# Kernel optimization log

Measured on AMD Instinct MI355X. Metric: run time of the kernel, lower is better.

The kernel has to match this reference:

```python
import jax, jax.numpy as jnp
import numpy as np


def _ln(x, g, b, eps=1e-5):
    m = jnp.mean(x, axis=-1, keepdims=True)
    v = jnp.mean(jnp.square(x - m), axis=-1, keepdims=True)
    return (x - m) * jax.lax.rsqrt(v + eps) * g + b


def setup_inputs() -> dict:
    N, F, H = 1024, 256, 64
    key = jax.random.key(0)
    ks = jax.random.split(key, 24)
    r = lambda k, s, sc=0.05: jax.random.normal(k, s, jnp.float32) * sc
    return {
        "features": jax.random.normal(ks[0], (N, F), jnp.float32),
        "ip_w1": r(ks[1], (F, H)), "ip_b1": r(ks[2], (H,)),
        "ip_ln_g": jnp.ones((H,), jnp.float32), "ip_ln_b": jnp.zeros((H,), jnp.float32),
        "ip_w2": r(ks[3], (H, H)), "ip_b2": r(ks[4], (H,)),
        "attn_in_w": r(ks[5], (H, 3 * H)), "attn_in_b": r(ks[6], (3 * H,)),
        "attn_out_w": r(ks[7], (H, H)), "attn_out_b": r(ks[8], (H,)),
        "attn_ln_g": jnp.ones((H,), jnp.float32), "attn_ln_b": jnp.zeros((H,), jnp.float32),
        "pg_w1": r(ks[9], (4 * H, H)), "pg_b1": r(ks[10], (H,)),
        "pg_w2": r(ks[11], (H, 1)), "pg_b2": r(ks[12], (1,)),
        "pv_w1": r(ks[13], (4 * H, H)), "pv_b1": r(ks[14], (H,)),
        "pv_w2": r(ks[15], (H, H)), "pv_b2": r(ks[16], (H,)),
        "ctx_ln_g": jnp.ones((H,), jnp.float32), "ctx_ln_b": jnp.zeros((H,), jnp.float32),
        "sh_w1": r(ks[17], (2 * H, H)), "sh_b1": r(ks[18], (H,)),
        "sh_w2": r(ks[19], (H, 1)), "sh_b2": r(ks[20], (1,)),
    }


def reference(features, ip_w1, ip_b1, ip_ln_g, ip_ln_b, ip_w2, ip_b2,
              attn_in_w, attn_in_b, attn_out_w, attn_out_b, attn_ln_g, attn_ln_b,
              pg_w1, pg_b1, pg_w2, pg_b2, pv_w1, pv_b1, pv_w2, pv_b2,
              ctx_ln_g, ctx_ln_b, sh_w1, sh_b1, sh_w2, sh_b2):
    N = features.shape[0]
    H = ip_w1.shape[1]
    NH = 4
    HD = H // NH
    # input_proj: Linear -> LayerNorm -> ReLU -> Linear -> ReLU
    h = jax.nn.relu(_ln(features @ ip_w1 + ip_b1, ip_ln_g, ip_ln_b))
    h = jax.nn.relu(h @ ip_w2 + ip_b2)
    # MultiheadAttention (batch=1, seq=N) with residual + LayerNorm
    qkv = h @ attn_in_w + attn_in_b
    q, k, v = jnp.split(qkv, 3, axis=-1)
    q = q.reshape(N, NH, HD)
    k = k.reshape(N, NH, HD)
    v = v.reshape(N, NH, HD)
    scores = jnp.einsum('ihd,jhd->hij', q, k) / np.sqrt(HD)
    attn = jax.nn.softmax(scores, axis=-1)
    o = jnp.einsum('hij,jhd->ihd', attn, v).reshape(N, H) @ attn_out_w + attn_out_b
    enc = _ln(h + o, attn_ln_g, attn_ln_b)
    # dense all-pairs gated message passing
    lhs = jnp.broadcast_to(enc[:, None, :], (N, N, H))
    rhs = jnp.broadcast_to(enc[None, :, :], (N, N, H))
    diff = lhs - rhs
    pf = jnp.concatenate([lhs, rhs, diff, jnp.abs(diff)], axis=-1)  # [N, N, 4H]
    gates = (jax.nn.relu(pf @ pg_w1 + pg_b1) @ pg_w2 + pg_b2)[..., 0]  # [N, N]
    gates = jnp.where(jnp.eye(N, dtype=bool), jnp.float32(-1e9), gates)
    w = jax.nn.softmax(gates, axis=1)
    vals = jax.nn.relu(pf @ pv_w1 + pv_b1) @ pv_w2 + pv_b2  # [N, N, H]
    pair_context = jnp.einsum('ij,ijh->ih', w, vals)
    enc2 = _ln(enc + pair_context, ctx_ln_g, ctx_ln_b)
    # score head with mean graph context
    g = jnp.broadcast_to(jnp.mean(enc2, axis=0, keepdims=True), (N, H))
    cat = jnp.concatenate([enc2, g], axis=-1)
    return (jax.nn.relu(cat @ sh_w1 + sh_b1) @ sh_w2 + sh_b2)[..., 0]  # [N]
```

## Files before the change

kernel.cpp:

```cpp
#include <hip/hip_runtime.h>
#include <hip/hip_bf16.h>
#include <hip/hip_fp16.h>
#include <math.h>

#define N 1024
#define F 256
#define H 64

typedef __attribute__((ext_vector_type(8))) _Float16 f16x8;
typedef __attribute__((ext_vector_type(4))) unsigned int u32x4;
typedef __attribute__((ext_vector_type(4))) float f32x4;

__device__ __forceinline__ float wave_reduce_sum(float v) {
#pragma unroll
  for (int off = 32; off; off >>= 1) v += __shfl_xor(v, off, 64);
  return v;
}

__device__ __forceinline__ unsigned int hpack(float a, float b) {
  __half ha = __float2half(a), hb = __float2half(b);
  unsigned short ua = __builtin_bit_cast(unsigned short, ha);
  unsigned short ub = __builtin_bit_cast(unsigned short, hb);
  return (unsigned int)ua | ((unsigned int)ub << 16);
}

__device__ __forceinline__ unsigned int absdiff2(unsigned int a, unsigned int b) {
  __half2 ah = __builtin_bit_cast(__half2, a);
  __half2 bh = __builtin_bit_cast(__half2, b);
  __half2 d = __hsub2(ah, bh);
  return __builtin_bit_cast(unsigned int, d) & 0x7FFF7FFFu;
}

__global__ void k_input_qkv(const float* __restrict__ feat,
                            const float* __restrict__ w1, const float* __restrict__ b1,
                            const float* __restrict__ lng, const float* __restrict__ lnb,
                            const float* __restrict__ w2, const float* __restrict__ b2,
                            const float* __restrict__ aw, const float* __restrict__ abias,
                            float* __restrict__ h, float* __restrict__ Qh,
                            float* __restrict__ Kh, float* __restrict__ Vh) {
  const int row = blockIdx.x;
  const int lane = threadIdx.x;
  __shared__ float frow[F];
#pragma unroll
  for (int c = 0; c < 4; ++c) frow[c * 64 + lane] = feat[row * F + c * 64 + lane];
  __syncthreads();
  float acc = b1[lane];
#pragma unroll 8
  for (int k = 0; k < F; ++k) acc += frow[k] * w1[k * H + lane];
  float mu = wave_reduce_sum(acc) * (1.f / 64.f);
  float d = acc - mu;
  float var = wave_reduce_sum(d * d) * (1.f / 64.f);
  float y = d * rsqrtf(var + 1e-5f) * lng[lane] + lnb[lane];
  y = fmaxf(y, 0.f);
  __shared__ float yrow[H];
  yrow[lane] = y;
  __syncthreads();
  float acc2 = b2[lane];
#pragma unroll 8
  for (int k = 0; k < H; ++k) acc2 += yrow[k] * w2[k * H + lane];
  float hv = fmaxf(acc2, 0.f);
  h[row * H + lane] = hv;
  __shared__ float hrow[H];
  hrow[lane] = hv;
  __syncthreads();
  float a0 = abias[lane], a1 = abias[64 + lane], a2 = abias[128 + lane];
#pragma unroll 8
  for (int k = 0; k < H; ++k) {
    float hk = hrow[k];
    a0 += hk * aw[k * 192 + lane];
    a1 += hk * aw[k * 192 + 64 + lane];
    a2 += hk * aw[k * 192 + 128 + lane];
  }
  const int base = (lane >> 4) * (N * 16) + row * 16 + (lane & 15);
  Qh[base] = a0;
  Kh[base] = a1;
  Vh[base] = a2;
}

__global__ __launch_bounds__(256) void k_attn2(const float* __restrict__ Qh,
                                               const float* __restrict__ Kh,
                                               const float* __restrict__ Vh,
                                               float* __restrict__ o) {
  const int head = blockIdx.x >> 8;
  const int i0 = (blockIdx.x & 255) * 4;
  const int tid = threadIdx.x;
  const int q2 = tid >> 6, js = tid & 63;
  const int i = i0 + q2;

  const float* qp = Qh + head * (N * 16) + i * 16;
  const float4 q0 = *(const float4*)(qp);
  const float4 q1 = *(const float4*)(qp + 4);
  const float4 q2v = *(const float4*)(qp + 8);
  const float4 q3 = *(const float4*)(qp + 12);
  const float* kb = Kh + head * (N * 16);
  const float* vb = Vh + head * (N * 16);

  float m = -3.0e38f, s = 0.f;
  float4 c0 = {0, 0, 0, 0}, c1 = {0, 0, 0, 0}, c2 = {0, 0, 0, 0}, c3 = {0, 0, 0, 0};

  int j = js;
  const float* kp = kb + j * 16;
  const float* vp = vb + j * 16;
  float4 k0 = *(const float4*)(kp), k1 = *(const float4*)(kp + 4);
  float4 k2 = *(const float4*)(kp + 8), k3 = *(const float4*)(kp + 12);
  float4 v0 = *(const float4*)(vp), v1 = *(const float4*)(vp + 4);
  float4 v2 = *(const float4*)(vp + 8), v3 = *(const float4*)(vp + 12);

#pragma unroll 1
  for (int t = 0; t < 16; ++t) {
    const int jn = (j + 64) & (N - 1);
    const float* kpn = kb + jn * 16;
    const float* vpn = vb + jn * 16;
    float4 nk0 = *(const float4*)(kpn), nk1 = *(const float4*)(kpn + 4);
    float4 nk2 = *(const float4*)(kpn + 8), nk3 = *(const float4*)(kpn + 12);
    float4 nv0 = *(const float4*)(vpn), nv1 = *(const float4*)(vpn + 4);
    float4 nv2 = *(const float4*)(vpn + 8), nv3 = *(const float4*)(vpn + 12);

    float sc = q0.x * k0.x + q0.y * k0.y + q0.z * k0.z + q0.w * k0.w;
    sc += q1.x * k1.x + q1.y * k1.y + q1.z * k1.z + q1.w * k1.w;
    sc += q2v.x * k2.x + q2v.y * k2.y + q2v.z * k2.z + q2v.w * k2.w;
    sc += q3.x * k3.x + q3.y * k3.y + q3.z * k3.z + q3.w * k3.w;
    sc *= 0.25f;

    float mn = fmaxf(m, sc);
    float cc = __expf(m - mn);
    float p = __expf(sc - mn);
    s = s * cc + p;
    m = mn;
    c0.x = c0.x * cc + p * v0.x; c0.y = c0.y * cc + p * v0.y;
    c0.z = c0.z * cc + p * v0.z; c0.w = c0.w * cc + p * v0.w;
    c1.x = c1.x * cc + p * v1.x; c1.y = c1.y * cc + p * v1.y;
    c1.z = c1.z * cc + p * v1.z; c1.w = c1.w * cc + p * v1.w;
    c2.x = c2.x * cc + p * v2.x; c2.y = c2.y * cc + p * v2.y;
    c2.z = c2.z * cc + p * v2.z; c2.w = c2.w * cc + p * v2.w;
    c3.x = c3.x * cc + p * v3.x; c3.y = c3.y * cc + p * v3.y;
    c3.z = c3.z * cc + p * v3.z; c3.w = c3.w * cc + p * v3.w;

    k0 = nk0; k1 = nk1; k2 = nk2; k3 = nk3;
    v0 = nv0; v1 = nv1; v2 = nv2; v3 = nv3;
    j = jn;
  }

  float M = m, S = s;
#pragma unroll
  for (int off = 32; off; off >>= 1) {
    float Mo = __shfl_xor(M, off, 64);
    float So = __shfl_xor(S, off, 64);
    float Mn = fmaxf(M, Mo);
    S = S * __expf(M - Mn) + So * __expf(Mo - Mn);
    M = Mn;
  }
  const float wgt = __expf(m - M) / S;

  __shared__ float lds[4][64][17];
  float* lp = &lds[q2][js][0];
  lp[0] = c0.x * wgt;  lp[1] = c0.y * wgt;  lp[2] = c0.z * wgt;  lp[3] = c0.w * wgt;
  lp[4] = c1.x * wgt;  lp[5] = c1.y * wgt;  lp[6] = c1.z * wgt;  lp[7] = c1.w * wgt;
  lp[8] = c2.x * wgt;  lp[9] = c2.y * wgt;  lp[10] = c2.z * wgt; lp[11] = c2.w * wgt;
  lp[12] = c3.x * wgt; lp[13] = c3.y * wgt; lp[14] = c3.z * wgt; lp[15] = c3.w * wgt;
  __syncthreads();

  if (tid < 64) {
    const int q = tid >> 4, d = tid & 15;
    float sum = 0.f;
#pragma unroll
    for (int k = 0; k < 64; ++k) sum += lds[q][k][d];
    o[(i0 + q) * H + head * 16 + d] = sum;
  }
}

__global__ void k_attn_out(const float* __restrict__ o, const float* __restrict__ w,
                           const float* __restrict__ b, const float* __restrict__ h,
                           const float* __restrict__ lng, const float* __restrict__ lnb,
                           float* __restrict__ enc) {
  const int row = blockIdx.x;
  const int lane = threadIdx.x;
  __shared__ float orow[H];
  orow[lane] = o[row * H + lane];
  __syncthreads();
  float a = b[lane];
#pragma unroll 8
  for (int k = 0; k < H; ++k) a += orow[k] * w[k * H + lane];
  float x = h[row * H + lane] + a;
  float mu = wave_reduce_sum(x) * (1.f / 64.f);
  float d = x - mu;
  float var = wave_reduce_sum(d * d) * (1.f / 64.f);
  enc[row * H + lane] = d * rsqrtf(var + 1e-5f) * lng[lane] + lnb[lane];
}

__global__ __launch_bounds__(256) void k_prep(const float* __restrict__ pg1,
                                              const float* __restrict__ pv1,
                                              float* __restrict__ WgA, float* __restrict__ WgB,
                                              float* __restrict__ WvA, float* __restrict__ WvB,
                                              unsigned int* __restrict__ WF) {
  const int blk = blockIdx.x;
  if (blk < 16) {
    int idx = blk * 256 + threadIdx.x;
    float g1 = pg1[idx];
    float g2 = pg1[4096 + idx];
    float g3 = pg1[8192 + idx];
    WgA[idx] = g1 + g3;
    WgB[idx] = g2 - g3;
    float v1 = pv1[idx];
    float v2 = pv1[4096 + idx];
    float v3 = pv1[8192 + idx];
    WvA[idx] = v1 + v3;
    WvB[idx] = v2 - v3;
  } else {
    const int sub = threadIdx.x >> 6;
    const int lane = threadIdx.x & 63;
    const int b = (blk - 16) * 4 + sub;
    const float* W = (b & 8) ? pv1 : pg1;
    const int Mt = b & 3;
    const int ks = (b >> 2) & 1;
    const int l = Mt * 16 + (lane & 15);
    const int kb = 192 + ks * 32 + (lane >> 4) * 8;
    uint4 o;
    o.x = hpack(W[(kb + 0) * H + l], W[(kb + 1) * H + l]);
    o.y = hpack(W[(kb + 2) * H + l], W[(kb + 3) * H + l]);
    o.z = hpack(W[(kb + 4) * H + l], W[(kb + 5) * H + l]);
    o.w = hpack(W[(kb + 6) * H + l], W[(kb + 7) * H + l]);
    ((uint4*)WF)[b * 64 + lane] = o;
  }
}

__global__ void k_ab(const float* __restrict__ enc, const float* __restrict__ WgA,
                     const float* __restrict__ WgB, const float* __restrict__ WvA,
                     const float* __restrict__ WvB, const float* __restrict__ pg_b1,
                     const float* __restrict__ pv_b1, float* __restrict__ Ag,
                     float* __restrict__ Av, float* __restrict__ Pg,
                     float* __restrict__ Pv, unsigned int* __restrict__ encH) {
  const int row = blockIdx.x;
  const int lane = threadIdx.x;
  __shared__ float erow[H];
  erow[lane] = enc[row * H + lane];
  __syncthreads();
  if (lane < 32) encH[row * 32 + lane] = hpack(erow[2 * lane], erow[2 * lane + 1]);
  float ag = pg_b1[lane], bg = 0.f, av = pv_b1[lane], bv = 0.f;
#pragma unroll 4
  for (int k = 0; k < H; ++k) {
    float e = erow[k];
    ag += e * WgA[k * H + lane];
    bg += e * WgB[k * H + lane];
    av += e * WvA[k * H + lane];
    bv += e * WvB[k * H + lane];
  }
  Ag[row * H + lane] = ag;
  Av[row * H + lane] = av;
  int idx = (((row >> 4) * 4 + (lane >> 4)) * 4 + ((lane >> 2) & 3)) * 64 +
            (row & 15) * 4 + (lane & 3);
  Pg[idx] = bg;
  Pv[idx] = bv;
}

__global__ __launch_bounds__(128) void k_pairp(
    const unsigned int* __restrict__ encH, const float* __restrict__ Ag,
    const float* __restrict__ Av, const unsigned int* __restrict__ WF,
    const float* __restrict__ Pg, const float* __restrict__ Pv,
    const float* __restrict__ pg_w2, const float* __restrict__ pg_b2,
    float* __restrict__ Pm, float* __restrict__ Ps,
    float* __restrict__ Pctx0, float* __restrict__ Pctx1) {
  const int bid = blockIdx.x;
  const int i = bid & (N - 1);
  const int half = bid >> 10;
  const int tid = threadIdx.x;
  const int lane = tid & 63;
  const int w = tid >> 6;
  const int l15 = lane & 15, g4 = lane >> 4;
  const float LOG2E = 1.44269504088896f;

  f16x8 wg[2][4], wv[2][4];
  const uint4* WF4 = (const uint4*)WF;
#pragma unroll
  for (int ks = 0; ks < 2; ++ks)
#pragma unroll
    for (int Mt = 0; Mt < 4; ++Mt) {
      wg[ks][Mt] = __builtin_bit_cast(f16x8, WF4[(ks * 4 + Mt) * 64 + lane]);
      wv[ks][Mt] = __builtin_bit_cast(f16x8, WF4[((2 + ks) * 4 + Mt) * 64 + lane]);
    }

  const uint4* eH = (const uint4*)encH + (size_t)i * 8;
  const uint4 eiL = eH[g4];
  const uint4 eiU = eH[4 + g4];

  f32x4 agv[4], avv[4];
  float4 w2s[4];
#pragma unroll
  for (int Mt = 0; Mt < 4; ++Mt) {
    float4 t = *(const float4*)(Ag + i * H + Mt * 16 + g4 * 4);
    agv[Mt] = f32x4{t.x, t.y, t.z, t.w};
    float4 u = *(const float4*)(Av + i * H + Mt * 16 + g4 * 4);
    avv[Mt] = f32x4{u.x, u.y, u.z, u.w};
    float4 ww = *(const float4*)(pg_w2 + Mt * 16 + g4 * 4);
    w2s[Mt] = make_float4(ww.x * LOG2E, ww.y * LOG2E, ww.z * LOG2E, ww.w * LOG2E);
  }
  const float b2g = pg_b2[0] * LOG2E;

  float m = -3.0e38f, s = 0.f;
  float ctx[16];
#pragma unroll
  for (int e = 0; e < 16; ++e) ctx[e] = 0.f;

  const int jbase = half * 512 + w * 256;
  const uint4* ejp = (const uint4*)encH + (size_t)(jbase + l15) * 8;
  uint4 na = ejp[g4];
  uint4 nc = ejp[4 + g4];

#pragma unroll 1
  for (int t = 0; t < 16; ++t) {
    const int j0 = jbase + t * 16;
    const int pbase = ((j0 >> 4) * 16 + g4) * 64 + l15 * 4;
    float4 pg0 = *(const float4*)(Pg + pbase);
    float4 pg1 = *(const float4*)(Pg + pbase + 256);
    float4 pg2 = *(const float4*)(Pg + pbase + 512);
    float4 pg3 = *(const float4*)(Pg + pbase + 768);

    u32x4 t0 = {absdiff2(eiL.x, na.x), absdiff2(eiL.y, na.y),
                absdiff2(eiL.z, na.z), absdiff2(eiL.w, na.w)};
    u32x4 t1 = {absdiff2(eiU.x, nc.x), absdiff2(eiU.y, nc.y),
                absdiff2(eiU.z, nc.z), absdiff2(eiU.w, nc.w)};
    f16x8 b0 = __builtin_bit_cast(f16x8, t0);
    f16x8 b1 = __builtin_bit_cast(f16x8, t1);
    ejp += 16 * 8;
    na = ejp[g4];
    nc = ejp[4 + g4];

    f32x4 cg[4], cv[4];
#pragma unroll
    for (int Mt = 0; Mt < 4; ++Mt) {
      cg[Mt] = __builtin_amdgcn_mfma_f32_16x16x32_f16(wg[0][Mt], b0, agv[Mt], 0, 0, 0);
      cg[Mt] = __builtin_amdgcn_mfma_f32_16x16x32_f16(wg[1][Mt], b1, cg[Mt], 0, 0, 0);
      cv[Mt] = __builtin_amdgcn_mfma_f32_16x16x32_f16(wv[0][Mt], b0, avv[Mt], 0, 0, 0);
      cv[Mt] = __builtin_amdgcn_mfma_f32_16x16x32_f16(wv[1][Mt], b1, cv[Mt], 0, 0, 0);
    }

    float4 pv0 = *(const float4*)(Pv + pbase);
    float4 pv1 = *(const float4*)(Pv + pbase + 256);
    float4 pv2 = *(const float4*)(Pv + pbase + 512);
    float4 pv3 = *(const float4*)(Pv + pbase + 768);

    float ga = fmaxf(cg[0][0] + pg0.x, 0.f) * w2s[0].x;
    float gb = fmaxf(cg[0][1] + pg0.y, 0.f) * w2s[0].y;
    float gc = fmaxf(cg[0][2] + pg0.z, 0.f) * w2s[0].z;
    float gd = fmaxf(cg[0][3] + pg0.w, 0.f) * w2s[0].w;
    ga = fmaf(fmaxf(cg[1][0] + pg1.x, 0.f), w2s[1].x, ga);
    gb = fmaf(fmaxf(cg[1][1] + pg1.y, 0.f), w2s[1].y, gb);
    gc = fmaf(fmaxf(cg[1][2] + pg1.z, 0.f), w2s[1].z, gc);
    gd = fmaf(fmaxf(cg[1][3] + pg1.w, 0.f), w2s[1].w, gd);
    ga = fmaf(fmaxf(cg[2][0] + pg2.x, 0.f), w2s[2].x, ga);
    gb = fmaf(fmaxf(cg[2][1] + pg2.y, 0.f), w2s[2].y, gb);
    gc = fmaf(fmaxf(cg[2][2] + pg2.z, 0.f), w2s[2].z, gc);
    gd = fmaf(fmaxf(cg[2][3] + pg2.w, 0.f), w2s[2].w, gd);
    ga = fmaf(fmaxf(cg[3][0] + pg3.x, 0.f), w2s[3].x, ga);
    gb = fmaf(fmaxf(cg[3][1] + pg3.y, 0.f), w2s[3].y, gb);
    gc = fmaf(fmaxf(cg[3][2] + pg3.z, 0.f), w2s[3].z, gc);
    gd = fmaf(fmaxf(cg[3][3] + pg3.w, 0.f), w2s[3].w, gd);
    float gate = (ga + gb) + (gc + gd);
    gate += __shfl_xor(gate, 16, 64);
    gate += __shfl_xor(gate, 32, 64);
    gate += b2g;
    if (j0 + l15 == i) gate = -3.0e38f;

    float p;
    if (__any(gate > m + 8.f)) {
      float mn = fmaxf(m, gate);
      float c = exp2f(m - mn);
      p = exp2f(gate - mn);
      s *= c;
      m = mn;
#pragma unroll
      for (int e = 0; e < 16; ++e) ctx[e] *= c;
    } else {
      p = exp2f(gate - m);
    }
    s += p;
    ctx[0]  = fmaf(p, fmaxf(cv[0][0] + pv0.x, 0.f), ctx[0]);
    ctx[1]  = fmaf(p, fmaxf(cv[0][1] + pv0.y, 0.f), ctx[1]);
    ctx[2]  = fmaf(p, fmaxf(cv[0][2] + pv0.z, 0.f), ctx[2]);
    ctx[3]  = fmaf(p, fmaxf(cv[0][3] + pv0.w, 0.f), ctx[3]);
    ctx[4]  = fmaf(p, fmaxf(cv[1][0] + pv1.x, 0.f), ctx[4]);
    ctx[5]  = fmaf(p, fmaxf(cv[1][1] + pv1.y, 0.f), ctx[5]);
    ctx[6]  = fmaf(p, fmaxf(cv[1][2] + pv1.z, 0.f), ctx[6]);
    ctx[7]  = fmaf(p, fmaxf(cv[1][3] + pv1.w, 0.f), ctx[7]);
    ctx[8]  = fmaf(p, fmaxf(cv[2][0] + pv2.x, 0.f), ctx[8]);
    ctx[9]  = fmaf(p, fmaxf(cv[2][1] + pv2.y, 0.f), ctx[9]);
    ctx[10] = fmaf(p, fmaxf(cv[2][2] + pv2.z, 0.f), ctx[10]);
    ctx[11] = fmaf(p, fmaxf(cv[2][3] + pv2.w, 0.f), ctx[11]);
    ctx[12] = fmaf(p, fmaxf(cv[3][0] + pv3.x, 0.f), ctx[12]);
    ctx[13] = fmaf(p, fmaxf(cv[3][1] + pv3.y, 0.f), ctx[13]);
    ctx[14] = fmaf(p, fmaxf(cv[3][2] + pv3.z, 0.f), ctx[14]);
    ctx[15] = fmaf(p, fmaxf(cv[3][3] + pv3.w, 0.f), ctx[15]);
  }

#pragma unroll
  for (int off = 1; off <= 8; off <<= 1) {
    float mo = __shfl_xor(m, off, 64);
    float so = __shfl_xor(s, off, 64);
    float M2 = fmaxf(m, mo);
    float ca = exp2f(m - M2);
    float cb = exp2f(mo - M2);
    s = s * ca + so * cb;
#pragma unroll
    for (int e = 0; e < 16; ++e) {
      float co = __shfl_xor(ctx[e], off, 64);
      ctx[e] = ctx[e] * ca + co * cb;
    }
    m = M2;
  }

  __shared__ float ctxs[2][64];
  __shared__ float mss[2][2];
  if (l15 == 0) {
#pragma unroll
    for (int Mt = 0; Mt < 4; ++Mt)
#pragma unroll
      for (int r = 0; r < 4; ++r) ctxs[w][Mt * 16 + g4 * 4 + r] = ctx[Mt * 4 + r];
  }
  if (lane == 0) {
    mss[w][0] = m;
    mss[w][1] = s;
  }
  __syncthreads();

  if (w == 0) {
    float m0 = mss[0][0], s0 = mss[0][1], m1 = mss[1][0], s1 = mss[1][1];
    float M = fmaxf(m0, m1);
    float e0 = exp2f(m0 - M), e1 = exp2f(m1 - M);
    float S = s0 * e0 + s1 * e1;
    float cm = ctxs[0][lane] * e0 + ctxs[1][lane] * e1;
    float* dst = half ? Pctx1 : Pctx0;
    dst[i * H + lane] = cm;
    if (lane == 0) {
      Pm[bid] = M;
      Ps[bid] = S;
    }
  }
}

__global__ void k_pmerge(const float* __restrict__ Pm, const float* __restrict__ Ps,
                         const float* __restrict__ Pctx0, const float* __restrict__ Pctx1,
                         const float* __restrict__ enc, const float* __restrict__ pv_w2,
                         const float* __restrict__ pv_b2, const float* __restrict__ lng,
                         const float* __restrict__ lnb, float* __restrict__ enc2) {
  const int i = blockIdx.x;
  const int lane = threadIdx.x;
  float m0 = Pm[i], s0 = Ps[i], m1 = Pm[N + i], s1 = Ps[N + i];
  float c0 = Pctx0[i * H + lane];
  float c1 = Pctx1[i * H + lane];
  float M = fmaxf(m0, m1);
  float e0 = exp2f(m0 - M), e1 = exp2f(m1 - M);
  float S = s0 * e0 + s1 * e1;
  float cp = (c0 * e0 + c1 * e1) / S;
  float pc = pv_b2[lane];
#pragma unroll 8
  for (int k = 0; k < 64; ++k) pc += __shfl(cp, k, 64) * pv_w2[k * H + lane];
  float x = enc[i * H + lane] + pc;
  float mu = wave_reduce_sum(x) * (1.f / 64.f);
  float dd = x - mu;
  float var = wave_reduce_sum(dd * dd) * (1.f / 64.f);
  enc2[i * H + lane] = dd * rsqrtf(var + 1e-5f) * lng[lane] + lnb[lane];
}

__global__ __launch_bounds__(256) void k_colsum(const float* __restrict__ enc2,
                                                float* __restrict__ part) {
  const int b = blockIdx.x;
  const int lane = threadIdx.x & 63, grp = threadIdx.x >> 6;
  const float* p = enc2 + (b * 32 + grp) * H + lane;
  float s = 0.f;
#pragma unroll
  for (int r = 0; r < 8; ++r) s += p[r * 4 * H];
  __shared__ float sh[4][64];
  sh[grp][lane] = s;
  __syncthreads();
  if (grp == 0) part[b * 64 + lane] = sh[0][lane] + sh[1][lane] + sh[2][lane] + sh[3][lane];
}

__global__ void k_score(const float* __restrict__ enc2, const float* __restrict__ sh_w1,
                        const float* __restrict__ sh_b1, const float* __restrict__ sh_w2,
                        const float* __restrict__ sh_b2, const float* __restrict__ part,
                        float* __restrict__ out) {
  const int row = blockIdx.x;
  const int lane = threadIdx.x;
  __shared__ float erow[H];
  erow[lane] = enc2[row * H + lane];
  __syncthreads();
  float g = 0.f;
#pragma unroll
  for (int p = 0; p < 32; ++p) g += part[p * 64 + lane];
  g *= (1.f / N);
  float t = sh_b1[lane];
#pragma unroll 8
  for (int k = 0; k < 64; ++k) {
    t += erow[k] * sh_w1[k * H + lane];
    t += __shfl(g, k, 64) * sh_w1[(64 + k) * H + lane];
  }
  t = fmaxf(t, 0.f);
  float prt = t * sh_w2[lane];
  float sum = wave_reduce_sum(prt);
  if (lane == 0) out[row] = sum + sh_b2[0];
}

extern "C" void kernel_launch(void* const* d_in, const int* in_sizes, int n_in,
                              void* d_out, int out_size, void* d_ws, size_t ws_size,
                              hipStream_t stream) {
  const float* feat = (const float*)d_in[0];
  const float* ip_w1 = (const float*)d_in[1];
  const float* ip_b1 = (const float*)d_in[2];
  const float* ip_ln_g = (const float*)d_in[3];
  const float* ip_ln_b = (const float*)d_in[4];
  const float* ip_w2 = (const float*)d_in[5];
  const float* ip_b2 = (const float*)d_in[6];
  const float* attn_in_w = (const float*)d_in[7];
  const float* attn_in_b = (const float*)d_in[8];
  const float* attn_out_w = (const float*)d_in[9];
  const float* attn_out_b = (const float*)d_in[10];
  const float* attn_ln_g = (const float*)d_in[11];
  const float* attn_ln_b = (const float*)d_in[12];
  const float* pg_w1 = (const float*)d_in[13];
  const float* pg_b1 = (const float*)d_in[14];
  const float* pg_w2 = (const float*)d_in[15];
  const float* pg_b2 = (const float*)d_in[16];
  const float* pv_w1 = (const float*)d_in[17];
  const float* pv_b1 = (const float*)d_in[18];
  const float* pv_w2 = (const float*)d_in[19];
  const float* pv_b2 = (const float*)d_in[20];
  const float* ctx_ln_g = (const float*)d_in[21];
  const float* ctx_ln_b = (const float*)d_in[22];
  const float* sh_w1 = (const float*)d_in[23];
  const float* sh_b1 = (const float*)d_in[24];
  const float* sh_w2 = (const float*)d_in[25];
  const float* sh_b2 = (const float*)d_in[26];

  float* ws = (float*)d_ws;
  float* h = ws;
  float* Qh = ws + 65536;
  float* Kh = ws + 131072;
  float* Vh = ws + 196608;
  float* o = ws + 262144;
  float* enc = ws + 327680;
  float* enc2 = ws + 393216;
  float* Pg = ws + 65536;
  float* Pv = ws + 131072;
  float* Ag = ws + 196608;
  float* Av = ws + 262144;
  float* Pctx0 = ws;
  float* Pctx1 = enc2;
  float* WgA = ws + 458752;
  float* WgB = ws + 462848;
  float* WvA = ws + 466944;
  float* WvB = ws + 471040;
  unsigned int* WF = (unsigned int*)(ws + 475136);
  float* part = ws + 479232;
  float* Pm = ws + 481280;
  float* Ps = ws + 483328;
  unsigned int* encH = (unsigned int*)(ws + 485376);
  float* out = (float*)d_out;

  k_input_qkv<<<N, 64, 0, stream>>>(feat, ip_w1, ip_b1, ip_ln_g, ip_ln_b, ip_w2, ip_b2,
                                    attn_in_w, attn_in_b, h, Qh, Kh, Vh);
  k_attn2<<<1024, 256, 0, stream>>>(Qh, Kh, Vh, o);
  k_attn_out<<<N, 64, 0, stream>>>(o, attn_out_w, attn_out_b, h, attn_ln_g, attn_ln_b, enc);
  k_prep<<<20, 256, 0, stream>>>(pg_w1, pv_w1, WgA, WgB, WvA, WvB, WF);
  k_ab<<<N, 64, 0, stream>>>(enc, WgA, WgB, WvA, WvB, pg_b1, pv_b1, Ag, Av, Pg, Pv, encH);
  k_pairp<<<2 * N, 128, 0, stream>>>(encH, Ag, Av, WF, Pg, Pv, pg_w2, pg_b2, Pm, Ps,
                                     Pctx0, Pctx1);
  k_pmerge<<<N, 64, 0, stream>>>(Pm, Ps, Pctx0, Pctx1, enc, pv_w2, pv_b2, ctx_ln_g,
                                 ctx_ln_b, enc2);
  k_colsum<<<32, 256, 0, stream>>>(enc2, part);
  k_score<<<N, 64, 0, stream>>>(enc2, sh_w1, sh_b1, sh_w2, sh_b2, part, out);
}
```

Baseline: 107.8 us.

## Fuse small kernels, pack four rows per block, stage attention K/V in LDS

Merges the weight-prep kernel into the input/QKV kernel, attn_out into k_ab, and colsum into k_score, cutting the launch count from nine to six. The per-row kernels now run four rows per 256-thread block. The attention kernel stages K/V tiles through double-buffered shared memory instead of each thread loading its own rows from global memory. Each k_score block now recomputes the full column sum redundantly, and the workspace layout is remapped (Av and Pctx0 swap regions) to avoid overlaps.

```diff
diff --git a/kernel.cpp b/kernel.cpp
--- a/kernel.cpp
+++ b/kernel.cpp
@@ -31,42 +31,78 @@
   return __builtin_bit_cast(unsigned int, d) & 0x7FFF7FFFu;
 }
 
-__global__ void k_input_qkv(const float* __restrict__ feat,
-                            const float* __restrict__ w1, const float* __restrict__ b1,
-                            const float* __restrict__ lng, const float* __restrict__ lnb,
-                            const float* __restrict__ w2, const float* __restrict__ b2,
-                            const float* __restrict__ aw, const float* __restrict__ abias,
-                            float* __restrict__ h, float* __restrict__ Qh,
-                            float* __restrict__ Kh, float* __restrict__ Vh) {
-  const int row = blockIdx.x;
-  const int lane = threadIdx.x;
-  __shared__ float frow[F];
-#pragma unroll
-  for (int c = 0; c < 4; ++c) frow[c * 64 + lane] = feat[row * F + c * 64 + lane];
+__global__ __launch_bounds__(256) void k_input_qkv_prep(
+    const float* __restrict__ feat, const float* __restrict__ w1,
+    const float* __restrict__ b1, const float* __restrict__ lng,
+    const float* __restrict__ lnb, const float* __restrict__ w2,
+    const float* __restrict__ b2, const float* __restrict__ aw,
+    const float* __restrict__ abias, const float* __restrict__ pg1,
+    const float* __restrict__ pv1, float* __restrict__ h, float* __restrict__ Qh,
+    float* __restrict__ Kh, float* __restrict__ Vh, float* __restrict__ WgA,
+    float* __restrict__ WgB, float* __restrict__ WvA, float* __restrict__ WvB,
+    unsigned int* __restrict__ WF) {
+  if (blockIdx.x >= 256) {
+    const int pb = blockIdx.x - 256;
+    const int tid = threadIdx.x;
+#pragma unroll
+    for (int c = 0; c < 4; ++c) {
+      int idx = (pb * 4 + c) * 256 + tid;
+      float g1 = pg1[idx];
+      float g2 = pg1[4096 + idx];
+      float g3 = pg1[8192 + idx];
+      WgA[idx] = g1 + g3;
+      WgB[idx] = g2 - g3;
+      float v1 = pv1[idx];
+      float v2 = pv1[4096 + idx];
+      float v3 = pv1[8192 + idx];
+      WvA[idx] = v1 + v3;
+      WvB[idx] = v2 - v3;
+    }
+    const int sub = tid >> 6;
+    const int lane = tid & 63;
+    const int b = pb * 4 + sub;
+    const float* W = (b & 8) ? pv1 : pg1;
+    const int Mt = b & 3;
+    const int ks = (b >> 2) & 1;
+    const int l = Mt * 16 + (lane & 15);
+    const int kb = 192 + ks * 32 + (lane >> 4) * 8;
+    uint4 o;
+    o.x = hpack(W[(kb + 0) * H + l], W[(kb + 1) * H + l]);
+    o.y = hpack(W[(kb + 2) * H + l], W[(kb + 3) * H + l]);
+    o.z = hpack(W[(kb + 4) * H + l], W[(kb + 5) * H + l]);
+    o.w = hpack(W[(kb + 6) * H + l], W[(kb + 7) * H + l]);
+    ((uint4*)WF)[b * 64 + lane] = o;
+    return;
+  }
+  const int sub = threadIdx.x >> 6, lane = threadIdx.x & 63;
+  const int row = blockIdx.x * 4 + sub;
+  __shared__ float frow[4][F];
+#pragma unroll
+  for (int c = 0; c < 4; ++c) frow[sub][c * 64 + lane] = feat[row * F + c * 64 + lane];
   __syncthreads();
   float acc = b1[lane];
 #pragma unroll 8
-  for (int k = 0; k < F; ++k) acc += frow[k] * w1[k * H + lane];
+  for (int k = 0; k < F; ++k) acc += frow[sub][k] * w1[k * H + lane];
   float mu = wave_reduce_sum(acc) * (1.f / 64.f);
   float d = acc - mu;
   float var = wave_reduce_sum(d * d) * (1.f / 64.f);
   float y = d * rsqrtf(var + 1e-5f) * lng[lane] + lnb[lane];
   y = fmaxf(y, 0.f);
-  __shared__ float yrow[H];
-  yrow[lane] = y;
+  __shared__ float yrow[4][H];
+  yrow[sub][lane] = y;
   __syncthreads();
   float acc2 = b2[lane];
 #pragma unroll 8
-  for (int k = 0; k < H; ++k) acc2 += yrow[k] * w2[k * H + lane];
+  for (int k = 0; k < H; ++k) acc2 += yrow[sub][k] * w2[k * H + lane];
   float hv = fmaxf(acc2, 0.f);
   h[row * H + lane] = hv;
-  __shared__ float hrow[H];
-  hrow[lane] = hv;
+  __shared__ float hrow[4][H];
+  hrow[sub][lane] = hv;
   __syncthreads();
   float a0 = abias[lane], a1 = abias[64 + lane], a2 = abias[128 + lane];
 #pragma unroll 8
   for (int k = 0; k < H; ++k) {
-    float hk = hrow[k];
+    float hk = hrow[sub][k];
     a0 += hk * aw[k * 192 + lane];
     a1 += hk * aw[k * 192 + 64 + lane];
     a2 += hk * aw[k * 192 + 128 + lane];
@@ -95,26 +131,28 @@
   const float* kb = Kh + head * (N * 16);
   const float* vb = Vh + head * (N * 16);
 
+  __shared__ float4 kt[2][4][64];
+  __shared__ float4 vt[2][4][64];
+  const int sr = tid & 63, sg = tid >> 6;
+  kt[0][sg][sr] = *(const float4*)(kb + sr * 16 + sg * 4);
+  vt[0][sg][sr] = *(const float4*)(vb + sr * 16 + sg * 4);
+  __syncthreads();
+
   float m = -3.0e38f, s = 0.f;
   float4 c0 = {0, 0, 0, 0}, c1 = {0, 0, 0, 0}, c2 = {0, 0, 0, 0}, c3 = {0, 0, 0, 0};
 
-  int j = js;
-  const float* kp = kb + j * 16;
-  const float* vp = vb + j * 16;
-  float4 k0 = *(const float4*)(kp), k1 = *(const float4*)(kp + 4);
-  float4 k2 = *(const float4*)(kp + 8), k3 = *(const float4*)(kp + 12);
-  float4 v0 = *(const float4*)(vp), v1 = *(const float4*)(vp + 4);
-  float4 v2 = *(const float4*)(vp + 8), v3 = *(const float4*)(vp + 12);
-
 #pragma unroll 1
   for (int t = 0; t < 16; ++t) {
-    const int jn = (j + 64) & (N - 1);
-    const float* kpn = kb + jn * 16;
-    const float* vpn = vb + jn * 16;
-    float4 nk0 = *(const float4*)(kpn), nk1 = *(const float4*)(kpn + 4);
-    float4 nk2 = *(const float4*)(kpn + 8), nk3 = *(const float4*)(kpn + 12);
-    float4 nv0 = *(const float4*)(vpn), nv1 = *(const float4*)(vpn + 4);
-    float4 nv2 = *(const float4*)(vpn + 8), nv3 = *(const float4*)(vpn + 12);
+    const int cur = t & 1;
+    if (t < 15) {
+      const int jr = (t + 1) * 64 + sr;
+      kt[cur ^ 1][sg][sr] = *(const float4*)(kb + jr * 16 + sg * 4);
+      vt[cur ^ 1][sg][sr] = *(const float4*)(vb + jr * 16 + sg * 4);
+    }
+    const float4 k0 = kt[cur][0][js], k1 = kt[cur][1][js];
+    const float4 k2 = kt[cur][2][js], k3 = kt[cur][3][js];
+    const float4 v0 = vt[cur][0][js], v1 = vt[cur][1][js];
+    const float4 v2 = vt[cur][2][js], v3 = vt[cur][3][js];
 
     float sc = q0.x * k0.x + q0.y * k0.y + q0.z * k0.z + q0.w * k0.w;
     sc += q1.x * k1.x + q1.y * k1.y + q1.z * k1.z + q1.w * k1.w;
@@ -135,10 +173,7 @@
     c2.z = c2.z * cc + p * v2.z; c2.w = c2.w * cc + p * v2.w;
     c3.x = c3.x * cc + p * v3.x; c3.y = c3.y * cc + p * v3.y;
     c3.z = c3.z * cc + p * v3.z; c3.w = c3.w * cc + p * v3.w;
-
-    k0 = nk0; k1 = nk1; k2 = nk2; k3 = nk3;
-    v0 = nv0; v1 = nv1; v2 = nv2; v3 = nv3;
-    j = jn;
+    __syncthreads();
   }
 
   float M = m, S = s;
@@ -169,81 +204,41 @@
   }
 }
 
-__global__ void k_attn_out(const float* __restrict__ o, const float* __restrict__ w,
-                           const float* __restrict__ b, const float* __restrict__ h,
-                           const float* __restrict__ lng, const float* __restrict__ lnb,
-                           float* __restrict__ enc) {
-  const int row = blockIdx.x;
-  const int lane = threadIdx.x;
-  __shared__ float orow[H];
-  orow[lane] = o[row * H + lane];
+__global__ __launch_bounds__(256) void k_attn_ab(
+    const float* __restrict__ o, const float* __restrict__ w, const float* __restrict__ b,
+    const float* __restrict__ h, const float* __restrict__ lng,
+    const float* __restrict__ lnb, const float* __restrict__ WgA,
+    const float* __restrict__ WgB, const float* __restrict__ WvA,
+    const float* __restrict__ WvB, const float* __restrict__ pg_b1,
+    const float* __restrict__ pv_b1, float* __restrict__ enc, float* __restrict__ Ag,
+    float* __restrict__ Av, float* __restrict__ Pg, float* __restrict__ Pv,
+    unsigned int* __restrict__ encH) {
+  const int sub = threadIdx.x >> 6, lane = threadIdx.x & 63;
+  const int row = blockIdx.x * 4 + sub;
+  __shared__ float orow[4][H];
+  orow[sub][lane] = o[row * H + lane];
   __syncthreads();
   float a = b[lane];
 #pragma unroll 8
-  for (int k = 0; k < H; ++k) a += orow[k] * w[k * H + lane];
+  for (int k = 0; k < H; ++k) a += orow[sub][k] * w[k * H + lane];
   float x = h[row * H + lane] + a;
   float mu = wave_reduce_sum(x) * (1.f / 64.f);
   float d = x - mu;
   float var = wave_reduce_sum(d * d) * (1.f / 64.f);
-  enc[row * H + lane] = d * rsqrtf(var + 1e-5f) * lng[lane] + lnb[lane];
-}
-
-__global__ __launch_bounds__(256) void k_prep(const float* __restrict__ pg1,
-                                              const float* __restrict__ pv1,
-                                              float* __restrict__ WgA, float* __restrict__ WgB,
-                                              float* __restrict__ WvA, float* __restrict__ WvB,
-                                              unsigned int* __restrict__ WF) {
-  const int blk = blockIdx.x;
-  if (blk < 16) {
-    int idx = blk * 256 + threadIdx.x;
-    float g1 = pg1[idx];
-    float g2 = pg1[4096 + idx];
-    float g3 = pg1[8192 + idx];
-    WgA[idx] = g1 + g3;
-    WgB[idx] = g2 - g3;
-    float v1 = pv1[idx];
-    float v2 = pv1[4096 + idx];
-    float v3 = pv1[8192 + idx];
-    WvA[idx] = v1 + v3;
-    WvB[idx] = v2 - v3;
-  } else {
-    const int sub = threadIdx.x >> 6;
-    const int lane = threadIdx.x & 63;
-    const int b = (blk - 16) * 4 + sub;
-    const float* W = (b & 8) ? pv1 : pg1;
-    const int Mt = b & 3;
-    const int ks = (b >> 2) & 1;
-    const int l = Mt * 16 + (lane & 15);
-    const int kb = 192 + ks * 32 + (lane >> 4) * 8;
-    uint4 o;
-    o.x = hpack(W[(kb + 0) * H + l], W[(kb + 1) * H + l]);
-    o.y = hpack(W[(kb + 2) * H + l], W[(kb + 3) * H + l]);
-    o.z = hpack(W[(kb + 4) * H + l], W[(kb + 5) * H + l]);
-    o.w = hpack(W[(kb + 6) * H + l], W[(kb + 7) * H + l]);
-    ((uint4*)WF)[b * 64 + lane] = o;
-  }
-}
-
-__global__ void k_ab(const float* __restrict__ enc, const float* __restrict__ WgA,
-                     const float* __restrict__ WgB, const float* __restrict__ WvA,
-                     const float* __restrict__ WvB, const float* __restrict__ pg_b1,
-                     const float* __restrict__ pv_b1, float* __restrict__ Ag,
-                     float* __restrict__ Av, float* __restrict__ Pg,
-                     float* __restrict__ Pv, unsigned int* __restrict__ encH) {
-  const int row = blockIdx.x;
-  const int lane = threadIdx.x;
-  __shared__ float erow[H];
-  erow[lane] = enc[row * H + lane];
-  __syncthreads();
-  if (lane < 32) encH[row * 32 + lane] = hpack(erow[2 * lane], erow[2 * lane + 1]);
+  float e = d * rsqrtf(var + 1e-5f) * lng[lane] + lnb[lane];
+  enc[row * H + lane] = e;
+  __shared__ float erow[4][H];
+  erow[sub][lane] = e;
+  __syncthreads();
+  if (lane < 32) encH[row * 32 + lane] = hpack(erow[sub][2 * lane], erow[sub][2 * lane + 1]);
   float ag = pg_b1[lane], bg = 0.f, av = pv_b1[lane], bv = 0.f;
 #pragma unroll 4
   for (int k = 0; k < H; ++k) {
-    float e = erow[k];
-    ag += e * WgA[k * H + lane];
-    bg += e * WgB[k * H + lane];
-    av += e * WvA[k * H + lane];
-    bv += e * WvB[k * H + lane];
+    float ev = erow[sub][k];
+    ag += ev * WgA[k * H + lane];
+    bg += ev * WgB[k * H + lane];
+    av += ev * WvA[k * H + lane];
+    bv += ev * WvB[k * H + lane];
   }
   Ag[row * H + lane] = ag;
   Av[row * H + lane] = av;
@@ -437,13 +432,14 @@
   }
 }
 
-__global__ void k_pmerge(const float* __restrict__ Pm, const float* __restrict__ Ps,
-                         const float* __restrict__ Pctx0, const float* __restrict__ Pctx1,
-                         const float* __restrict__ enc, const float* __restrict__ pv_w2,
-                         const float* __restrict__ pv_b2, const float* __restrict__ lng,
-                         const float* __restrict__ lnb, float* __restrict__ enc2) {
-  const int i = blockIdx.x;
-  const int lane = threadIdx.x;
+__global__ __launch_bounds__(256) void k_pmerge(
+    const float* __restrict__ Pm, const float* __restrict__ Ps,
+    const float* __restrict__ Pctx0, const float* __restrict__ Pctx1,
+    const float* __restrict__ enc, const float* __restrict__ pv_w2,
+    const float* __restrict__ pv_b2, const float* __restrict__ lng,
+    const float* __restrict__ lnb, float* __restrict__ enc2) {
+  const int sub = threadIdx.x >> 6, lane = threadIdx.x & 63;
+  const int i = blockIdx.x * 4 + sub;
   float m0 = Pm[i], s0 = Ps[i], m1 = Pm[N + i], s1 = Ps[N + i];
   float c0 = Pctx0[i * H + lane];
   float c1 = Pctx1[i * H + lane];
@@ -461,37 +457,26 @@
   enc2[i * H + lane] = dd * rsqrtf(var + 1e-5f) * lng[lane] + lnb[lane];
 }
 
-__global__ __launch_bounds__(256) void k_colsum(const float* __restrict__ enc2,
-                                                float* __restrict__ part) {
-  const int b = blockIdx.x;
-  const int lane = threadIdx.x & 63, grp = threadIdx.x >> 6;
-  const float* p = enc2 + (b * 32 + grp) * H + lane;
-  float s = 0.f;
-#pragma unroll
-  for (int r = 0; r < 8; ++r) s += p[r * 4 * H];
-  __shared__ float sh[4][64];
-  sh[grp][lane] = s;
-  __syncthreads();
-  if (grp == 0) part[b * 64 + lane] = sh[0][lane] + sh[1][lane] + sh[2][lane] + sh[3][lane];
-}
-
-__global__ void k_score(const float* __restrict__ enc2, const float* __restrict__ sh_w1,
-                        const float* __restrict__ sh_b1, const float* __restrict__ sh_w2,
-                        const float* __restrict__ sh_b2, const float* __restrict__ part,
-                        float* __restrict__ out) {
-  const int row = blockIdx.x;
-  const int lane = threadIdx.x;
-  __shared__ float erow[H];
-  erow[lane] = enc2[row * H + lane];
-  __syncthreads();
-  float g = 0.f;
-#pragma unroll
-  for (int p = 0; p < 32; ++p) g += part[p * 64 + lane];
-  g *= (1.f / N);
+__global__ __launch_bounds__(256) void k_score(
+    const float* __restrict__ enc2, const float* __restrict__ sh_w1,
+    const float* __restrict__ sh_b1, const float* __restrict__ sh_w2,
+    const float* __restrict__ sh_b2, float* __restrict__ out) {
+  const int sub = threadIdx.x >> 6, lane = threadIdx.x & 63;
+  const int row = blockIdx.x * 4 + sub;
+  float cs = 0.f;
+  const float* pp = enc2 + (sub * 256) * H + lane;
+#pragma unroll 8
+  for (int r = 0; r < 256; ++r) cs += pp[r * H];
+  __shared__ float part[4][64];
+  __shared__ float erow[4][H];
+  part[sub][lane] = cs;
+  erow[sub][lane] = enc2[row * H + lane];
+  __syncthreads();
+  float g = (part[0][lane] + part[1][lane] + part[2][lane] + part[3][lane]) * (1.f / N);
   float t = sh_b1[lane];
 #pragma unroll 8
   for (int k = 0; k < 64; ++k) {
-    t += erow[k] * sh_w1[k * H + lane];
+    t += erow[sub][k] * sh_w1[k * H + lane];
     t += __shfl(g, k, 64) * sh_w1[(64 + k) * H + lane];
   }
   t = fmaxf(t, 0.f);
@@ -542,30 +527,29 @@
   float* Pg = ws + 65536;
   float* Pv = ws + 131072;
   float* Ag = ws + 196608;
-  float* Av = ws + 262144;
-  float* Pctx0 = ws;
+  float* Av = ws;
+  float* Pctx0 = ws + 262144;
   float* Pctx1 = enc2;
   float* WgA = ws + 458752;
   float* WgB = ws + 462848;
   float* WvA = ws + 466944;
   float* WvB = ws + 471040;
   unsigned int* WF = (unsigned int*)(ws + 475136);
-  float* part = ws + 479232;
-  float* Pm = ws + 481280;
-  float* Ps = ws + 483328;
-  unsigned int* encH = (unsigned int*)(ws + 485376);
+  float* Pm = ws + 479232;
+  float* Ps = ws + 481280;
+  unsigned int* encH = (unsigned int*)(ws + 483328);
   float* out = (float*)d_out;
 
-  k_input_qkv<<<N, 64, 0, stream>>>(feat, ip_w1, ip_b1, ip_ln_g, ip_ln_b, ip_w2, ip_b2,
-                                    attn_in_w, attn_in_b, h, Qh, Kh, Vh);
+  k_input_qkv_prep<<<260, 256, 0, stream>>>(feat, ip_w1, ip_b1, ip_ln_g, ip_ln_b, ip_w2,
+                                            ip_b2, attn_in_w, attn_in_b, pg_w1, pv_w1, h,
+                                            Qh, Kh, Vh, WgA, WgB, WvA, WvB, WF);
   k_attn2<<<1024, 256, 0, stream>>>(Qh, Kh, Vh, o);
-  k_attn_out<<<N, 64, 0, stream>>>(o, attn_out_w, attn_out_b, h, attn_ln_g, attn_ln_b, enc);
-  k_prep<<<20, 256, 0, stream>>>(pg_w1, pv_w1, WgA, WgB, WvA, WvB, WF);
-  k_ab<<<N, 64, 0, stream>>>(enc, WgA, WgB, WvA, WvB, pg_b1, pv_b1, Ag, Av, Pg, Pv, encH);
+  k_attn_ab<<<256, 256, 0, stream>>>(o, attn_out_w, attn_out_b, h, attn_ln_g, attn_ln_b,
+                                     WgA, WgB, WvA, WvB, pg_b1, pv_b1, enc, Ag, Av, Pg,
+                                     Pv, encH);
   k_pairp<<<2 * N, 128, 0, stream>>>(encH, Ag, Av, WF, Pg, Pv, pg_w2, pg_b2, Pm, Ps,
                                      Pctx0, Pctx1);
-  k_pmerge<<<N, 64, 0, stream>>>(Pm, Ps, Pctx0, Pctx1, enc, pv_w2, pv_b2, ctx_ln_g,
-                                 ctx_ln_b, enc2);
-  k_colsum<<<32, 256, 0, stream>>>(enc2, part);
-  k_score<<<N, 64, 0, stream>>>(enc2, sh_w1, sh_b1, sh_w2, sh_b2, part, out);
-}
+  k_pmerge<<<256, 256, 0, stream>>>(Pm, Ps, Pctx0, Pctx1, enc, pv_w2, pv_b2, ctx_ln_g,
+                                    ctx_ln_b, enc2);
+  k_score<<<256, 256, 0, stream>>>(enc2, sh_w1, sh_b1, sh_w2, sh_b2, out);
+}
```

Result: faster. 94.87 us (-12.0%).
